# Optimization experiments

Measured on AMD Instinct MI355X. Metric: run time of the kernel, lower is better.

The kernel has to match this reference:

```python
import jax, jax.numpy as jnp
import numpy as np
from jax import lax

# Module constants (from init_kwargs)
IN_FEATURES = 4096
OUT_FEATURES = 11008
TD_X = 16
TD_Y = 16
IN_PART = (2048, 2048)
L = 16
KV = (4, 4)
V = 2
TLUT_BITS = 9


def _decode_trellis(trellis, tlut, m, k_part, kv):
    """Bitshift-trellis decode of a compressed weight partition.

    trellis: [nb, nw] int32 holding 16-bit words (nb = (m/td_x)*(k_part/td_y)).
    Each step consumes kv bits, updating an L-bit sliding state; the low
    tlut_bits of the state index the LUT, yielding V weights per step.
    Returns dense weights [m, k_part].
    """
    nb, nw = trellis.shape
    steps = (TD_X * TD_Y) // V  # codes per block
    cpw = 16 // kv  # chunks per 16-bit word (kv divides 16)
    words = trellis.astype(jnp.int32) & 0xFFFF
    shifts = 16 - kv * (jnp.arange(cpw, dtype=jnp.int32) + 1)  # big-endian in word
    chunks = (words[:, :, None] >> shifts[None, None, :]) & ((1 << kv) - 1)
    chunks = chunks.reshape(nb, nw * cpw)[:, :steps]  # [nb, steps]

    l_mask = (1 << L) - 1
    t_mask = (1 << TLUT_BITS) - 1

    def step(state, c):
        state = ((state << kv) | c) & l_mask
        return state, state & t_mask

    _, idx = lax.scan(step, jnp.zeros((nb,), jnp.int32), chunks.T)  # [steps, nb]
    vals = tlut[idx]  # [steps, nb, V]
    blocks = vals.transpose(1, 0, 2).reshape(nb, TD_X, TD_Y)
    mo, ko = m // TD_X, k_part // TD_Y
    return blocks.reshape(mo, ko, TD_X, TD_Y).transpose(0, 2, 1, 3).reshape(m, k_part)


def setup_inputs() -> dict:
    key = jax.random.key(0)
    k1, k2, k3, k4 = jax.random.split(key, 4)
    nb = (OUT_FEATURES // TD_X) * (IN_PART[0] // TD_Y)
    nw = (TD_X * TD_Y * KV[0]) // 16 // V
    inp = jax.random.normal(k1, (4, IN_FEATURES), dtype=jnp.float32)
    trellis1 = jax.random.randint(k2, (nb, nw), 0, 65536, dtype=jnp.int32)
    trellis2 = jax.random.randint(k3, (nb, nw), 0, 65536, dtype=jnp.int32)
    tlut = jax.random.normal(k4, (2 ** TLUT_BITS, V), dtype=jnp.float32)
    return {"inp": inp, "trellis1": trellis1, "trellis2": trellis2, "tlut": tlut}


def reference(inp, trellis1, trellis2, tlut):
    x = inp.reshape(-1, IN_FEATURES)
    w1 = _decode_trellis(trellis1, tlut, OUT_FEATURES, IN_PART[0], KV[0])  # [m, k1]
    w2 = _decode_trellis(trellis2, tlut, OUT_FEATURES, IN_PART[1], KV[1])  # [m, k2]
    out = x[:, : IN_PART[0]] @ w1.T + x[:, IN_PART[0]:] @ w2.T  # [bs, m]
    return out.reshape(*inp.shape[:-1], OUT_FEATURES).astype(inp.dtype)
```

## Files before the change

### kernel.cpp

```cpp
#include <hip/hip_runtime.h>

#define IN_FEATURES 4096
#define OUT_FEATURES 11008
#define KO 128
#define NW 32
#define SEG 8
#define KO_PER_SEG (KO / SEG)

__global__ __launch_bounds__(256) void tcq_kernel(
    const float* __restrict__ inp,
    const int* __restrict__ trellis1,
    const int* __restrict__ trellis2,
    const float* __restrict__ tlut,
    float* __restrict__ out)
{
    __shared__ float lut[1024];
    {
        const float4* src = reinterpret_cast<const float4*>(tlut);
        float4* dst = reinterpret_cast<float4*>(lut);
        dst[threadIdx.x] = src[threadIdx.x];
    }
    __syncthreads();

    const int tid  = threadIdx.x;
    const int lane = tid & 63;
    const int wid  = tid >> 6;
    const int tx   = lane & 15;
    const int mt   = lane >> 4;
    const int mo   = blockIdx.x * 16 + wid * 4 + mt;
    const int m    = mo * 16 + tx;
    const int ko0  = blockIdx.y * KO_PER_SEG;
    const int part = blockIdx.z;

    const int* __restrict__ tre =
        (part ? trellis2 : trellis1) + (mo * KO + ko0) * NW;
    const float* __restrict__ xbase = inp + part * 2048 + ko0 * 16;

    float accE[4] = {0.f, 0.f, 0.f, 0.f};
    float accO[4] = {0.f, 0.f, 0.f, 0.f};

    for (int kk = 0; kk < KO_PER_SEG; ++kk) {
        const int* blk = tre + kk * NW;
        int2 wp = *reinterpret_cast<const int2*>(blk + 2 * tx);
        int wm1 = tx ? blk[2 * tx - 1] : 0;
        unsigned comb0 = (unsigned(wm1) << 16) | (unsigned(wp.x) & 0xFFFFu);
        unsigned comb1 = (unsigned(wp.x) << 16) | (unsigned(wp.y) & 0xFFFFu);

        const float* xt = xbase + kk * 16;
        float xs[4][16];
        #pragma unroll
        for (int b = 0; b < 4; ++b) {
            const float4* xv = reinterpret_cast<const float4*>(xt + b * IN_FEATURES);
            #pragma unroll
            for (int q = 0; q < 4; ++q) {
                float4 v = xv[q];
                xs[b][q * 4 + 0] = v.x;
                xs[b][q * 4 + 1] = v.y;
                xs[b][q * 4 + 2] = v.z;
                xs[b][q * 4 + 3] = v.w;
            }
        }

        #pragma unroll
        for (int j = 0; j < 8; ++j) {
            unsigned comb = (j < 4) ? comb0 : comb1;
            const int shift = 12 - 4 * (j & 3);
            unsigned idx = (comb >> shift) & 0x1FFu;
            float w0 = lut[idx * 2];
            float w1 = lut[idx * 2 + 1];
            #pragma unroll
            for (int b = 0; b < 4; ++b) {
                accE[b] = fmaf(w0, xs[b][2 * j],     accE[b]);
                accO[b] = fmaf(w1, xs[b][2 * j + 1], accO[b]);
            }
        }
    }

    #pragma unroll
    for (int b = 0; b < 4; ++b) {
        atomicAdd(&out[b * OUT_FEATURES + m], accE[b] + accO[b]);
    }
}

extern "C" void kernel_launch(void* const* d_in, const int* in_sizes, int n_in,
                              void* d_out, int out_size, void* d_ws, size_t ws_size,
                              hipStream_t stream) {
    const float* inp  = (const float*)d_in[0];
    const int*   t1   = (const int*)d_in[1];
    const int*   t2   = (const int*)d_in[2];
    const float* tlut = (const float*)d_in[3];
    float* out = (float*)d_out;

    hipMemsetAsync(out, 0, (size_t)out_size * sizeof(float), stream);

    dim3 grid(43, SEG, 2);
    dim3 block(256);
    hipLaunchKernelGGL(tcq_kernel, grid, block, 0, stream,
                       inp, t1, t2, tlut, out);
}
```

Measured before the change: 86.05 us.

## Stage activations in transposed LDS, prefetch trellis words, and double K segments

The activation slice for each block is now staged once in shared memory in transposed [k][batch] layout, so each step needs one float4 LDS read instead of per-thread global float4 loads. Trellis words for the next block are loaded one iteration ahead so global latency overlaps with decode and FMA work. The K dimension is split into 16 segments instead of 8, which doubles the grid and the number of atomic adds but shortens each thread's loop. LUT weight pairs are fetched as a single float2.

```diff
diff --git a/kernel.cpp b/kernel.cpp
--- a/kernel.cpp
+++ b/kernel.cpp
@@ -4,8 +4,9 @@
 #define OUT_FEATURES 11008
 #define KO 128
 #define NW 32
-#define SEG 8
+#define SEG 16
 #define KO_PER_SEG (KO / SEG)
+#define SEGK (KO_PER_SEG * 16)
 
 __global__ __launch_bounds__(256) void tcq_kernel(
     const float* __restrict__ inp,
@@ -15,71 +16,71 @@
     float* __restrict__ out)
 {
     __shared__ float lut[1024];
-    {
-        const float4* src = reinterpret_cast<const float4*>(tlut);
-        float4* dst = reinterpret_cast<float4*>(lut);
-        dst[threadIdx.x] = src[threadIdx.x];
+    __shared__ float xT[SEGK * 4];
+
+    const int tid  = threadIdx.x;
+    const int part = blockIdx.z;
+    const int ko0  = blockIdx.y * KO_PER_SEG;
+    const float* __restrict__ xbase = inp + part * 2048 + ko0 * 16;
+
+    ((float4*)lut)[tid] = ((const float4*)tlut)[tid];
+    if (tid < SEGK) {
+        #pragma unroll
+        for (int b = 0; b < 4; ++b)
+            xT[tid * 4 + b] = xbase[b * IN_FEATURES + tid];
     }
     __syncthreads();
 
-    const int tid  = threadIdx.x;
     const int lane = tid & 63;
     const int wid  = tid >> 6;
     const int tx   = lane & 15;
     const int mt   = lane >> 4;
     const int mo   = blockIdx.x * 16 + wid * 4 + mt;
     const int m    = mo * 16 + tx;
-    const int ko0  = blockIdx.y * KO_PER_SEG;
-    const int part = blockIdx.z;
 
     const int* __restrict__ tre =
         (part ? trellis2 : trellis1) + (mo * KO + ko0) * NW;
-    const float* __restrict__ xbase = inp + part * 2048 + ko0 * 16;
 
     float accE[4] = {0.f, 0.f, 0.f, 0.f};
     float accO[4] = {0.f, 0.f, 0.f, 0.f};
 
+    int2 wp  = *reinterpret_cast<const int2*>(tre + 2 * tx);
+    int  wm1 = tx ? tre[2 * tx - 1] : 0;
+
+    #pragma unroll
     for (int kk = 0; kk < KO_PER_SEG; ++kk) {
-        const int* blk = tre + kk * NW;
-        int2 wp = *reinterpret_cast<const int2*>(blk + 2 * tx);
-        int wm1 = tx ? blk[2 * tx - 1] : 0;
-        unsigned comb0 = (unsigned(wm1) << 16) | (unsigned(wp.x) & 0xFFFFu);
-        unsigned comb1 = (unsigned(wp.x) << 16) | (unsigned(wp.y) & 0xFFFFu);
-
-        const float* xt = xbase + kk * 16;
-        float xs[4][16];
-        #pragma unroll
-        for (int b = 0; b < 4; ++b) {
-            const float4* xv = reinterpret_cast<const float4*>(xt + b * IN_FEATURES);
-            #pragma unroll
-            for (int q = 0; q < 4; ++q) {
-                float4 v = xv[q];
-                xs[b][q * 4 + 0] = v.x;
-                xs[b][q * 4 + 1] = v.y;
-                xs[b][q * 4 + 2] = v.z;
-                xs[b][q * 4 + 3] = v.w;
-            }
+        int2 wp_n = wp; int wm1_n = 0;
+        if (kk + 1 < KO_PER_SEG) {
+            const int* nb = tre + (kk + 1) * NW;
+            wp_n  = *reinterpret_cast<const int2*>(nb + 2 * tx);
+            wm1_n = tx ? nb[2 * tx - 1] : 0;
         }
+        const unsigned comb0 = (unsigned(wm1)  << 16) | (unsigned(wp.x) & 0xFFFFu);
+        const unsigned comb1 = (unsigned(wp.x) << 16) | (unsigned(wp.y) & 0xFFFFu);
 
         #pragma unroll
         for (int j = 0; j < 8; ++j) {
-            unsigned comb = (j < 4) ? comb0 : comb1;
-            const int shift = 12 - 4 * (j & 3);
-            unsigned idx = (comb >> shift) & 0x1FFu;
-            float w0 = lut[idx * 2];
-            float w1 = lut[idx * 2 + 1];
-            #pragma unroll
-            for (int b = 0; b < 4; ++b) {
-                accE[b] = fmaf(w0, xs[b][2 * j],     accE[b]);
-                accO[b] = fmaf(w1, xs[b][2 * j + 1], accO[b]);
-            }
+            const unsigned comb  = (j < 4) ? comb0 : comb1;
+            const int      shift = 12 - 4 * (j & 3);
+            const unsigned idx   = (comb >> shift) & 0x1FFu;
+            float2 w  = *reinterpret_cast<const float2*>(&lut[idx * 2]);
+            float4 xa = *reinterpret_cast<const float4*>(&xT[(kk * 16 + 2 * j) * 4]);
+            float4 xb = *reinterpret_cast<const float4*>(&xT[(kk * 16 + 2 * j + 1) * 4]);
+            accE[0] = fmaf(w.x, xa.x, accE[0]);
+            accE[1] = fmaf(w.x, xa.y, accE[1]);
+            accE[2] = fmaf(w.x, xa.z, accE[2]);
+            accE[3] = fmaf(w.x, xa.w, accE[3]);
+            accO[0] = fmaf(w.y, xb.x, accO[0]);
+            accO[1] = fmaf(w.y, xb.y, accO[1]);
+            accO[2] = fmaf(w.y, xb.z, accO[2]);
+            accO[3] = fmaf(w.y, xb.w, accO[3]);
         }
+        wp = wp_n; wm1 = wm1_n;
     }
 
     #pragma unroll
-    for (int b = 0; b < 4; ++b) {
+    for (int b = 0; b < 4; ++b)
         atomicAdd(&out[b * OUT_FEATURES + m], accE[b] + accO[b]);
-    }
 }
 
 extern "C" void kernel_launch(void* const* d_in, const int* in_sizes, int n_in,
```

New measurement: 103.0 us. +19.7%, slower.

## Split K into more segments and reduce partials via workspace instead of atomics

Applied to the files above, without the earlier changes.

Raises the K-split from 8 to 32 segments, which quadruples the number of workgroups, and adds an occupancy hint to the launch bounds. Each workgroup now writes its partial sums to a workspace buffer. A second kernel then sums the 64 partials per output, replacing the memset and the float atomics. This is meant to improve parallelism and avoid atomic contention, at the cost of about 11 MB of workspace traffic and an extra kernel launch.

```diff
diff --git a/kernel.cpp b/kernel.cpp
--- a/kernel.cpp
+++ b/kernel.cpp
@@ -4,22 +4,19 @@
 #define OUT_FEATURES 11008
 #define KO 128
 #define NW 32
-#define SEG 8
+#define SEG 32
 #define KO_PER_SEG (KO / SEG)
+#define NPART (SEG * 2)
 
-__global__ __launch_bounds__(256) void tcq_kernel(
+__global__ __launch_bounds__(256, 6) void tcq_decode_kernel(
     const float* __restrict__ inp,
     const int* __restrict__ trellis1,
     const int* __restrict__ trellis2,
     const float* __restrict__ tlut,
-    float* __restrict__ out)
+    float* __restrict__ ws)
 {
     __shared__ float lut[1024];
-    {
-        const float4* src = reinterpret_cast<const float4*>(tlut);
-        float4* dst = reinterpret_cast<float4*>(lut);
-        dst[threadIdx.x] = src[threadIdx.x];
-    }
+    ((float4*)lut)[threadIdx.x] = ((const float4*)tlut)[threadIdx.x];
     __syncthreads();
 
     const int tid  = threadIdx.x;
@@ -29,56 +26,64 @@
     const int mt   = lane >> 4;
     const int mo   = blockIdx.x * 16 + wid * 4 + mt;
     const int m    = mo * 16 + tx;
-    const int ko0  = blockIdx.y * KO_PER_SEG;
+    const int seg  = blockIdx.y;
     const int part = blockIdx.z;
+    const int ko0  = seg * KO_PER_SEG;
 
     const int* __restrict__ tre =
         (part ? trellis2 : trellis1) + (mo * KO + ko0) * NW;
-    const float* __restrict__ xbase = inp + part * 2048 + ko0 * 16;
+    const float* __restrict__ xk = inp + part * 2048 + ko0 * 16;
 
     float accE[4] = {0.f, 0.f, 0.f, 0.f};
     float accO[4] = {0.f, 0.f, 0.f, 0.f};
 
+    #pragma unroll 1
     for (int kk = 0; kk < KO_PER_SEG; ++kk) {
         const int* blk = tre + kk * NW;
-        int2 wp = *reinterpret_cast<const int2*>(blk + 2 * tx);
-        int wm1 = tx ? blk[2 * tx - 1] : 0;
-        unsigned comb0 = (unsigned(wm1) << 16) | (unsigned(wp.x) & 0xFFFFu);
-        unsigned comb1 = (unsigned(wp.x) << 16) | (unsigned(wp.y) & 0xFFFFu);
+        int2 wp  = *reinterpret_cast<const int2*>(blk + 2 * tx);
+        int  wm1 = tx ? blk[2 * tx - 1] : 0;
+        const unsigned comb0 = (unsigned(wm1)  << 16) | (unsigned(wp.x) & 0xFFFFu);
+        const unsigned comb1 = (unsigned(wp.x) << 16) | (unsigned(wp.y) & 0xFFFFu);
 
-        const float* xt = xbase + kk * 16;
-        float xs[4][16];
+        float sx[4][16];
         #pragma unroll
         for (int b = 0; b < 4; ++b) {
-            const float4* xv = reinterpret_cast<const float4*>(xt + b * IN_FEATURES);
             #pragma unroll
-            for (int q = 0; q < 4; ++q) {
-                float4 v = xv[q];
-                xs[b][q * 4 + 0] = v.x;
-                xs[b][q * 4 + 1] = v.y;
-                xs[b][q * 4 + 2] = v.z;
-                xs[b][q * 4 + 3] = v.w;
-            }
+            for (int q = 0; q < 16; ++q)
+                sx[b][q] = xk[b * IN_FEATURES + kk * 16 + q];
         }
 
         #pragma unroll
         for (int j = 0; j < 8; ++j) {
-            unsigned comb = (j < 4) ? comb0 : comb1;
-            const int shift = 12 - 4 * (j & 3);
-            unsigned idx = (comb >> shift) & 0x1FFu;
-            float w0 = lut[idx * 2];
-            float w1 = lut[idx * 2 + 1];
+            const unsigned comb  = (j < 4) ? comb0 : comb1;
+            const int      shift = 12 - 4 * (j & 3);
+            const unsigned idx   = (comb >> shift) & 0x1FFu;
+            float2 w = *reinterpret_cast<const float2*>(&lut[idx * 2]);
             #pragma unroll
             for (int b = 0; b < 4; ++b) {
-                accE[b] = fmaf(w0, xs[b][2 * j],     accE[b]);
-                accO[b] = fmaf(w1, xs[b][2 * j + 1], accO[b]);
+                accE[b] = fmaf(w.x, sx[b][2 * j],     accE[b]);
+                accO[b] = fmaf(w.y, sx[b][2 * j + 1], accO[b]);
             }
         }
     }
 
+    float* wsp = ws + (size_t)(part * SEG + seg) * 4 * OUT_FEATURES;
     #pragma unroll
-    for (int b = 0; b < 4; ++b) {
-        atomicAdd(&out[b * OUT_FEATURES + m], accE[b] + accO[b]);
+    for (int b = 0; b < 4; ++b)
+        wsp[b * OUT_FEATURES + m] = accE[b] + accO[b];
+}
+
+__global__ __launch_bounds__(256) void tcq_reduce_kernel(
+    const float* __restrict__ ws,
+    float* __restrict__ out)
+{
+    const int i = blockIdx.x * 256 + threadIdx.x;
+    if (i < 4 * OUT_FEATURES) {
+        float s = 0.f;
+        #pragma unroll
+        for (int p = 0; p < NPART; ++p)
+            s += ws[(size_t)p * 4 * OUT_FEATURES + i];
+        out[i] = s;
     }
 }
 
@@ -90,11 +95,13 @@
     const int*   t2   = (const int*)d_in[2];
     const float* tlut = (const float*)d_in[3];
     float* out = (float*)d_out;
+    float* ws  = (float*)d_ws;
 
-    hipMemsetAsync(out, 0, (size_t)out_size * sizeof(float), stream);
+    dim3 grid1(43, SEG, 2);
+    hipLaunchKernelGGL(tcq_decode_kernel, grid1, dim3(256), 0, stream,
+                       inp, t1, t2, tlut, ws);
 
-    dim3 grid(43, SEG, 2);
-    dim3 block(256);
-    hipLaunchKernelGGL(tcq_kernel, grid, block, 0, stream,
-                       inp, t1, t2, tlut, out);
+    dim3 grid2((4 * OUT_FEATURES + 255) / 256);
+    hipLaunchKernelGGL(tcq_reduce_kernel, grid2, dim3(256), 0, stream,
+                       ws, out);
 }
```

Result: slower. 96.90 us (+12.6%).
